# Performance work log

Measured on AMD Instinct MI355X. Metric: run time of the kernel, lower is better.

Reference implementation:

```python
import jax, jax.numpy as jnp
import numpy as np

N = 50000
E = 800000
IN_C, HID_C, OUT_C = 128, 256, 2


def sage_conv(x, src, dst, W_l, b_l, W_r, num_nodes):
    # PyG SAGEConv with mean aggregation:
    #   out = lin_l(mean_{j in N(i)} x_j) + lin_r(x_i)
    msg = x[src]                                            # [E, d] gather
    agg = jax.ops.segment_sum(msg, dst, num_segments=num_nodes)   # [N, d]
    cnt = jax.ops.segment_sum(jnp.ones((msg.shape[0],), x.dtype), dst,
                              num_segments=num_nodes)        # [N]
    agg = agg / jnp.maximum(cnt, 1.0)[:, None]               # mean (deg>=1)
    return agg @ W_l.T + b_l + x @ W_r.T


def setup_inputs() -> dict:
    key = jax.random.key(0)
    ks = jax.random.split(key, 8)
    x = jax.random.normal(ks[0], (N, IN_C), dtype=jnp.float32)
    edge_index = jax.random.randint(ks[1], (2, E), 0, N, dtype=jnp.int32)
    # glorot-ish scaled params
    s1 = 1.0 / np.sqrt(IN_C)
    s2 = 1.0 / np.sqrt(HID_C)
    W1l = jax.random.normal(ks[2], (HID_C, IN_C), dtype=jnp.float32) * s1
    W1r = jax.random.normal(ks[3], (HID_C, IN_C), dtype=jnp.float32) * s1
    b1 = jnp.zeros((HID_C,), dtype=jnp.float32)
    W2l = jax.random.normal(ks[4], (OUT_C, HID_C), dtype=jnp.float32) * s2
    W2r = jax.random.normal(ks[5], (OUT_C, HID_C), dtype=jnp.float32) * s2
    b2 = jnp.zeros((OUT_C,), dtype=jnp.float32)
    return {"x": x, "edge_index": edge_index,
            "W1l": W1l, "b1": b1, "W1r": W1r,
            "W2l": W2l, "b2": b2, "W2r": W2r}


def reference(x, edge_index, W1l, b1, W1r, W2l, b2, W2r):
    src, dst = edge_index[0], edge_index[1]
    h = sage_conv(x, src, dst, W1l, b1, W1r, N)
    h = jax.nn.relu(h)
    out = sage_conv(h, src, dst, W2l, b2, W2r, N)
    return out
```

## Files before the change

### kernel.cpp

```cpp
#include <hip/hip_runtime.h>
#include <hip/hip_bf16.h>


#define IN_C 128
#define HID_C 256
#define BKT_SHIFT 7
#define BKT_W 128
#define MAX_BKT_E 4096

typedef __attribute__((ext_vector_type(8))) short short8;
typedef __attribute__((ext_vector_type(4))) float f32x4;

static __device__ __forceinline__ unsigned short f2b(float f) {
    __hip_bfloat16 h = __float2bfloat16(f);
    return *(unsigned short*)&h;
}
static __device__ __forceinline__ float b2f(unsigned short u) {
    unsigned v = ((unsigned)u) << 16;
    return *(float*)&v;
}


__global__ __launch_bounds__(256) void bin_count(const int* __restrict__ ei,
                                                 int* __restrict__ bhist, int E_) {
    __shared__ int hist[512];
    const int tid = threadIdx.x;
    for (int i = tid; i < 512; i += 256) hist[i] = 0;
    __syncthreads();
    const int e0 = blockIdx.x * 2048;
#pragma unroll
    for (int j = 0; j < 8; ++j) {
        int e = e0 + j * 256 + tid;
        if (e < E_) atomicAdd(&hist[ei[E_ + e] >> BKT_SHIFT], 1);
    }
    __syncthreads();
    for (int i = tid; i < 512; i += 256) {
        int c = hist[i];
        if (c) atomicAdd(&bhist[i], c);
    }
}

__global__ __launch_bounds__(512) void bin_scan(const int* __restrict__ bhist,
                                                int* __restrict__ bbase,
                                                int* __restrict__ bcursor,
                                                int* __restrict__ rowptr,
                                                int nbkt, int n, int E_) {
    __shared__ int wsum[8];
    const int tid = threadIdx.x;
    const int lane = tid & 63;
    const int wid = tid >> 6;
    int v = (tid < nbkt) ? bhist[tid] : 0;
    int incl = v;
#pragma unroll
    for (int off = 1; off < 64; off <<= 1) {
        int t = __shfl_up(incl, off);
        if (lane >= off) incl += t;
    }
    if (lane == 63) wsum[wid] = incl;
    __syncthreads();
    int woff = 0;
    for (int w = 0; w < 8; ++w)
        if (w < wid) woff += wsum[w];
    int excl = woff + incl - v;
    if (tid < nbkt) { bbase[tid] = excl; bcursor[tid] = excl; }
    if (tid == 511) { bbase[nbkt] = woff + incl; rowptr[n] = E_; }
}

__global__ __launch_bounds__(256) void bin_scatter(const int* __restrict__ ei,
                                                   int* __restrict__ bcursor,
                                                   unsigned int* __restrict__ binned,
                                                   int E_) {
    __shared__ int hist[512];
    __shared__ int lbase[512];
    const int tid = threadIdx.x;
    const int e0 = blockIdx.x * 4096;
    for (int i = tid; i < 512; i += 256) hist[i] = 0;
    __syncthreads();
#pragma unroll
    for (int j = 0; j < 16; ++j) {
        int e = e0 + j * 256 + tid;
        if (e < E_) atomicAdd(&hist[ei[E_ + e] >> BKT_SHIFT], 1);
    }
    __syncthreads();
    for (int i = tid; i < 512; i += 256) {
        int c = hist[i];
        lbase[i] = c ? atomicAdd(&bcursor[i], c) : 0;
        hist[i] = 0;
    }
    __syncthreads();
#pragma unroll
    for (int j = 0; j < 16; ++j) {
        int e = e0 + j * 256 + tid;
        if (e < E_) {
            int d = ei[E_ + e];
            int b = d >> BKT_SHIFT;
            int pos = lbase[b] + atomicAdd(&hist[b], 1);
            binned[pos] = ((unsigned)ei[e] << BKT_SHIFT) | (unsigned)(d & (BKT_W - 1));
        }
    }
}

__global__ __launch_bounds__(256) void fine_sort(const unsigned int* __restrict__ binned,
                                                 const int* __restrict__ bbase,
                                                 int* __restrict__ rowptr,
                                                 int* __restrict__ elist, int n) {
    __shared__ unsigned int ebuf[MAX_BKT_E];
    __shared__ unsigned short sbuf[MAX_BKT_E];
    __shared__ int hist[BKT_W];
    __shared__ int offs[BKT_W];
    __shared__ int cur[BKT_W];
    const int tid = threadIdx.x;
    const int lane = tid & 63;
    const int bkt = blockIdx.x;
    const int gbase = bbase[bkt];
    int cnt = bbase[bkt + 1] - gbase;
    if (cnt > MAX_BKT_E) cnt = MAX_BKT_E;

    if (tid < BKT_W) hist[tid] = 0;
    for (int i = tid; i < cnt; i += 256) ebuf[i] = binned[gbase + i];
    __syncthreads();
    for (int i = tid; i < cnt; i += 256)
        atomicAdd(&hist[ebuf[i] & (BKT_W - 1)], 1);
    __syncthreads();
    if (tid < 64) {
        int h0 = hist[lane * 2], h1 = hist[lane * 2 + 1];
        int s = h0 + h1;
        int incl = s;
#pragma unroll
        for (int off = 1; off < 64; off <<= 1) {
            int t = __shfl_up(incl, off);
            if (lane >= off) incl += t;
        }
        int excl = incl - s;
        offs[lane * 2] = excl;         cur[lane * 2] = excl;
        offs[lane * 2 + 1] = excl + h0; cur[lane * 2 + 1] = excl + h0;
    }
    __syncthreads();
    if (tid < BKT_W) {
        int d = bkt * BKT_W + tid;
        if (d < n) rowptr[d] = gbase + offs[tid];
    }
    for (int i = tid; i < cnt; i += 256) {
        unsigned int pk = ebuf[i];
        int pos = atomicAdd(&cur[pk & (BKT_W - 1)], 1);
        sbuf[pos] = (unsigned short)(pk >> BKT_SHIFT);
    }
    __syncthreads();
    for (int i = tid; i < cnt; i += 256)
        elist[gbase + i] = (int)sbuf[i];
}


__global__ void convert_all(const float* __restrict__ x, unsigned int* __restrict__ xh,
                            unsigned int* __restrict__ Abf,
                            const float* __restrict__ w1l, const float* __restrict__ w1r,
                            unsigned short* __restrict__ Bg,
                            int npairs , int xblk) {
    if (blockIdx.x < xblk) {
        int t = blockIdx.x * 256 + threadIdx.x;
        if (t >= npairs) return;
        float2 v = *(const float2*)&x[(size_t)t * 2];
        unsigned int o = ((unsigned)f2b(v.y) << 16) | f2b(v.x);
        xh[t] = o;
        int node = t >> 6, g = t & 63;
        Abf[(size_t)node * 128 + 64 + g] = o;
    } else {
        int idx = (blockIdx.x - xblk) * 256 + threadIdx.x;
        int o = idx >> 8, k = idx & 255;
        float f = (k < IN_C) ? w1l[o * IN_C + k] : w1r[o * IN_C + (k - IN_C)];
        Bg[idx] = f2b(f);
    }
}


__global__ __launch_bounds__(256) void gather_agg1(
    const int* __restrict__ rowptr, const int* __restrict__ elist,
    const uint4* __restrict__ xh4, uint4* __restrict__ Abf4, int n) {
    int node = blockIdx.x * 4 + (threadIdx.x >> 6);
    int lane = threadIdx.x & 63;
    if (node >= n) return;
    const int ep = lane >> 4;
    const int pos = lane & 15;
    int beg = rowptr[node], end = rowptr[node + 1];

    float s[8] = {0.f, 0.f, 0.f, 0.f, 0.f, 0.f, 0.f, 0.f};
    for (int e = beg; e < end; e += 8) {
        int e0 = e + ep;
        int e1 = e + 4 + ep;
        if (e0 < end) {
            uint4 u = xh4[(size_t)elist[e0] * 16 + pos];
            s[0] += b2f(u.x & 0xffff); s[1] += b2f(u.x >> 16);
            s[2] += b2f(u.y & 0xffff); s[3] += b2f(u.y >> 16);
            s[4] += b2f(u.z & 0xffff); s[5] += b2f(u.z >> 16);
            s[6] += b2f(u.w & 0xffff); s[7] += b2f(u.w >> 16);
        }
        if (e1 < end) {
            uint4 u = xh4[(size_t)elist[e1] * 16 + pos];
            s[0] += b2f(u.x & 0xffff); s[1] += b2f(u.x >> 16);
            s[2] += b2f(u.y & 0xffff); s[3] += b2f(u.y >> 16);
            s[4] += b2f(u.z & 0xffff); s[5] += b2f(u.z >> 16);
            s[6] += b2f(u.w & 0xffff); s[7] += b2f(u.w >> 16);
        }
    }
#pragma unroll
    for (int i = 0; i < 8; ++i) {
        s[i] += __shfl_xor(s[i], 16);
        s[i] += __shfl_xor(s[i], 32);
    }
    if (ep == 0) {
        float inv = 1.0f / (float)max(end - beg, 1);
        uint4 o;
        o.x = ((unsigned)f2b(s[1] * inv) << 16) | f2b(s[0] * inv);
        o.y = ((unsigned)f2b(s[3] * inv) << 16) | f2b(s[2] * inv);
        o.z = ((unsigned)f2b(s[5] * inv) << 16) | f2b(s[4] * inv);
        o.w = ((unsigned)f2b(s[7] * inv) << 16) | f2b(s[6] * inv);
        Abf4[(size_t)node * 32 + pos] = o;
    }
}


#define LSTR 72

__global__ __launch_bounds__(256) void gemm1_fused(
    const unsigned short* __restrict__ Abf, const unsigned short* __restrict__ Bg,
    const float* __restrict__ b1, const float* __restrict__ w2l,
    const float* __restrict__ w2r, float* __restrict__ pr_part, int nn) {
    __shared__ short As[128 * LSTR];
    __shared__ short Bs[128 * LSTR];

    const int tid = threadIdx.x;
    const int lane = tid & 63;
    const int wid = tid >> 6;
    const int wm = wid >> 1, wn = wid & 1;
    const int row0 = blockIdx.x * 128;
    const int col0 = blockIdx.y * 128;

    const int srow = tid >> 1;
    const int skc = (tid & 1) * 32;
    int arow = row0 + srow;
    if (arow >= nn) arow = nn - 1;
    const size_t agoff = (size_t)arow * 256 + skc;
    const size_t bgoff = (size_t)(col0 + srow) * 256 + skc;

    f32x4 acc[4][4];
#pragma unroll
    for (int i = 0; i < 4; ++i)
#pragma unroll
        for (int j = 0; j < 4; ++j) acc[i][j] = (f32x4){0.f, 0.f, 0.f, 0.f};

    const int quad = lane >> 4;
    const int l16 = lane & 15;

    for (int k0 = 0; k0 < 256; k0 += 64) {
        const uint4* ga = (const uint4*)(Abf + agoff + k0);
        const uint4* gb = (const uint4*)(Bg + bgoff + k0);
        uint4 va0 = ga[0], va1 = ga[1], va2 = ga[2], va3 = ga[3];
        uint4 vb0 = gb[0], vb1 = gb[1], vb2 = gb[2], vb3 = gb[3];

        __syncthreads();
        uint4* la = (uint4*)&As[srow * LSTR + skc];
        uint4* lb = (uint4*)&Bs[srow * LSTR + skc];
        la[0] = va0; la[1] = va1; la[2] = va2; la[3] = va3;
        lb[0] = vb0; lb[1] = vb1; lb[2] = vb2; lb[3] = vb3;
        __syncthreads();

#pragma unroll
        for (int kb = 0; kb < 2; ++kb) {
            short8 af[4], bf[4];
#pragma unroll
            for (int mt = 0; mt < 4; ++mt)
                af[mt] = *(const short8*)&As[(wm * 64 + mt * 16 + l16) * LSTR + kb * 32 + quad * 8];
#pragma unroll
            for (int nt = 0; nt < 4; ++nt)
                bf[nt] = *(const short8*)&Bs[(wn * 64 + nt * 16 + l16) * LSTR + kb * 32 + quad * 8];
#pragma unroll
            for (int mt = 0; mt < 4; ++mt)
#pragma unroll
                for (int nt = 0; nt < 4; ++nt)
                    acc[mt][nt] = __builtin_amdgcn_mfma_f32_16x16x32_bf16(
                        af[mt], bf[nt], acc[mt][nt], 0, 0, 0);
        }
    }

    const int cbase = col0 + wn * 64 + l16;
    const int cby = blockIdx.y * 2 + wn;
#pragma unroll
    for (int half = 0; half < 2; ++half) {
        const float* wA = half ? w2r : w2l;
        f32x4 part[2][4];
#pragma unroll
        for (int c = 0; c < 2; ++c)
#pragma unroll
            for (int mt = 0; mt < 4; ++mt) part[c][mt] = (f32x4){0.f, 0.f, 0.f, 0.f};
#pragma unroll
        for (int nt = 0; nt < 4; ++nt) {
            const int col = cbase + nt * 16;
            const float bias = b1[col];
            const float w0 = wA[col];
            const float w1 = wA[HID_C + col];
#pragma unroll
            for (int mt = 0; mt < 4; ++mt)
#pragma unroll
                for (int r = 0; r < 4; ++r) {
                    float hv = fmaxf(acc[mt][nt][r] + bias, 0.0f);
                    part[0][mt][r] += hv * w0;
                    part[1][mt][r] += hv * w1;
                }
        }
#pragma unroll
        for (int c = 0; c < 2; ++c)
#pragma unroll
            for (int mt = 0; mt < 4; ++mt)
#pragma unroll
                for (int r = 0; r < 4; ++r)
#pragma unroll
                    for (int m = 1; m < 16; m <<= 1)
                        part[c][mt][r] += __shfl_xor(part[c][mt][r], m);
        if (l16 < 8) {
            const int ch2 = l16 & 1;
            const int mts = l16 >> 1;
#pragma unroll
            for (int r = 0; r < 4; ++r) {
                int row = row0 + wm * 64 + quad * 4 + mts * 16 + r;
                if (row < nn)
                    pr_part[(size_t)row * 16 + cby * 4 + half * 2 + ch2] =
                        part[ch2][mts][r];
            }
        }
    }
}


__global__ void combine2(const float* __restrict__ pr_part,
                         float2* __restrict__ p2, float2* __restrict__ rs, int n) {
    int i = blockIdx.x * 256 + threadIdx.x;
    if (i >= n) return;
    const float4* q = (const float4*)(pr_part + (size_t)i * 16);
    float4 a = q[0], b = q[1], c = q[2], d = q[3];
    p2[i] = make_float2(a.x + b.x + c.x + d.x, a.y + b.y + c.y + d.y);
    rs[i] = make_float2(a.z + b.z + c.z + d.z, a.w + b.w + c.w + d.w);
}

__global__ void gather_fin(const int* __restrict__ rowptr, const int* __restrict__ elist,
                           const float2* __restrict__ p2, const float2* __restrict__ rs,
                           const float* __restrict__ b2, float* __restrict__ out, int n) {
    int i = blockIdx.x * 256 + threadIdx.x;
    if (i >= n) return;
    int beg = rowptr[i], end = rowptr[i + 1];
    float s0 = 0.0f, s1 = 0.0f;
    for (int e = beg; e < end; ++e) {
        float2 v = p2[elist[e]];
        s0 += v.x; s1 += v.y;
    }
    float inv = 1.0f / (float)max(end - beg, 1);
    float2 self = rs[i];
    out[i * 2 + 0] = s0 * inv + self.x + b2[0];
    out[i * 2 + 1] = s1 * inv + self.y + b2[1];
}


extern "C" void kernel_launch(void* const* d_in, const int* in_sizes, int n_in,
                              void* d_out, int out_size, void* d_ws, size_t ws_size,
                              hipStream_t stream) {
    const float* x   = (const float*)d_in[0];
    const int*   ei  = (const int*)d_in[1];
    const float* W1l = (const float*)d_in[2];
    const float* b1  = (const float*)d_in[3];
    const float* W1r = (const float*)d_in[4];
    const float* W2l = (const float*)d_in[5];
    const float* b2  = (const float*)d_in[6];
    const float* W2r = (const float*)d_in[7];
    float* out = (float*)d_out;

    const int N_ = in_sizes[0] / IN_C;
    const int E_ = in_sizes[1] / 2;
    const int nbkt = (N_ + BKT_W - 1) / BKT_W;

    char* wsb = (char*)d_ws;
    size_t off = 0;
    auto alloc = [&](size_t bytes) {
        void* ptr = wsb + off;
        off += ((bytes + 15) & ~(size_t)15);
        return ptr;
    };
    unsigned short* Abf = (unsigned short*)alloc((size_t)N_ * 256 * 2);
    unsigned int*   xh  = (unsigned int*)alloc((size_t)N_ * 64 * 4);
    unsigned short* Bg  = (unsigned short*)alloc(256 * 256 * 2);
    float* pr_part = (float*)alloc((size_t)N_ * 16 * 4);
    int*   rowptr = (int*)alloc((size_t)(N_ + 1) * 4);
    int*   elist  = (int*)alloc((size_t)E_ * 4);
    unsigned int* binned = (unsigned int*)alloc((size_t)E_ * 4);
    int*   bhist  = (int*)alloc(512 * 4);
    int*   bbase  = (int*)alloc(513 * 4);
    int*   bcursor= (int*)alloc(512 * 4);
    float2* p2 = (float2*)alloc((size_t)N_ * 2 * 4);
    float2* rs = (float2*)alloc((size_t)N_ * 2 * 4);

    const int xblk = (N_ * 64 + 255) / 256;

    hipMemsetAsync(bhist, 0, 512 * sizeof(int), stream);
    bin_count<<<(E_ + 2047) / 2048, 256, 0, stream>>>(ei, bhist, E_);
    convert_all<<<xblk + 256, 256, 0, stream>>>(x, xh, (unsigned int*)Abf,
                                                W1l, W1r, Bg, N_ * 64, xblk);
    bin_scan<<<1, 512, 0, stream>>>(bhist, bbase, bcursor, rowptr, nbkt, N_, E_);
    bin_scatter<<<(E_ + 4095) / 4096, 256, 0, stream>>>(ei, bcursor, binned, E_);
    fine_sort<<<nbkt, 256, 0, stream>>>(binned, bbase, rowptr, elist, N_);

    gather_agg1<<<(N_ + 3) / 4, 256, 0, stream>>>(rowptr, elist,
                                                  (const uint4*)xh, (uint4*)Abf, N_);
    gemm1_fused<<<dim3((N_ + 127) / 128, 2), 256, 0, stream>>>(
        Abf, Bg, b1, W2l, W2r, pr_part, N_);

    combine2<<<(N_ + 255) / 256, 256, 0, stream>>>(pr_part, p2, rs, N_);
    gather_fin<<<(N_ + 255) / 256, 256, 0, stream>>>(rowptr, elist, p2, rs, b2, out, N_);
}
```

Measured before the change: 219.3 us.

## Replace CSR fine sort with per-bucket shared-memory atomic aggregation

```diff
diff --git a/kernel.cpp b/kernel.cpp
--- a/kernel.cpp
+++ b/kernel.cpp
@@ -6,7 +6,6 @@
 #define HID_C 256
 #define BKT_SHIFT 7
 #define BKT_W 128
-#define MAX_BKT_E 4096
 
 typedef __attribute__((ext_vector_type(8))) short short8;
 typedef __attribute__((ext_vector_type(4))) float f32x4;
@@ -43,8 +42,7 @@
 __global__ __launch_bounds__(512) void bin_scan(const int* __restrict__ bhist,
                                                 int* __restrict__ bbase,
                                                 int* __restrict__ bcursor,
-                                                int* __restrict__ rowptr,
-                                                int nbkt, int n, int E_) {
+                                                int nbkt) {
     __shared__ int wsum[8];
     const int tid = threadIdx.x;
     const int lane = tid & 63;
@@ -63,7 +61,7 @@
         if (w < wid) woff += wsum[w];
     int excl = woff + incl - v;
     if (tid < nbkt) { bbase[tid] = excl; bcursor[tid] = excl; }
-    if (tid == 511) { bbase[nbkt] = woff + incl; rowptr[n] = E_; }
+    if (tid == 511) bbase[nbkt] = woff + incl;
 }
 
 __global__ __launch_bounds__(256) void bin_scatter(const int* __restrict__ ei,
@@ -98,56 +96,6 @@
             binned[pos] = ((unsigned)ei[e] << BKT_SHIFT) | (unsigned)(d & (BKT_W - 1));
         }
     }
-}
-
-__global__ __launch_bounds__(256) void fine_sort(const unsigned int* __restrict__ binned,
-                                                 const int* __restrict__ bbase,
-                                                 int* __restrict__ rowptr,
-                                                 int* __restrict__ elist, int n) {
-    __shared__ unsigned int ebuf[MAX_BKT_E];
-    __shared__ unsigned short sbuf[MAX_BKT_E];
-    __shared__ int hist[BKT_W];
-    __shared__ int offs[BKT_W];
-    __shared__ int cur[BKT_W];
-    const int tid = threadIdx.x;
-    const int lane = tid & 63;
-    const int bkt = blockIdx.x;
-    const int gbase = bbase[bkt];
-    int cnt = bbase[bkt + 1] - gbase;
-    if (cnt > MAX_BKT_E) cnt = MAX_BKT_E;
-
-    if (tid < BKT_W) hist[tid] = 0;
-    for (int i = tid; i < cnt; i += 256) ebuf[i] = binned[gbase + i];
-    __syncthreads();
-    for (int i = tid; i < cnt; i += 256)
-        atomicAdd(&hist[ebuf[i] & (BKT_W - 1)], 1);
-    __syncthreads();
-    if (tid < 64) {
-        int h0 = hist[lane * 2], h1 = hist[lane * 2 + 1];
-        int s = h0 + h1;
-        int incl = s;
-#pragma unroll
-        for (int off = 1; off < 64; off <<= 1) {
-            int t = __shfl_up(incl, off);
-            if (lane >= off) incl += t;
-        }
-        int excl = incl - s;
-        offs[lane * 2] = excl;         cur[lane * 2] = excl;
-        offs[lane * 2 + 1] = excl + h0; cur[lane * 2 + 1] = excl + h0;
-    }
-    __syncthreads();
-    if (tid < BKT_W) {
-        int d = bkt * BKT_W + tid;
-        if (d < n) rowptr[d] = gbase + offs[tid];
-    }
-    for (int i = tid; i < cnt; i += 256) {
-        unsigned int pk = ebuf[i];
-        int pos = atomicAdd(&cur[pk & (BKT_W - 1)], 1);
-        sbuf[pos] = (unsigned short)(pk >> BKT_SHIFT);
-    }
-    __syncthreads();
-    for (int i = tid; i < cnt; i += 256)
-        elist[gbase + i] = (int)sbuf[i];
 }
 
 
@@ -173,48 +121,57 @@
 }
 
 
-__global__ __launch_bounds__(256) void gather_agg1(
-    const int* __restrict__ rowptr, const int* __restrict__ elist,
-    const uint4* __restrict__ xh4, uint4* __restrict__ Abf4, int n) {
-    int node = blockIdx.x * 4 + (threadIdx.x >> 6);
-    int lane = threadIdx.x & 63;
-    if (node >= n) return;
-    const int ep = lane >> 4;
-    const int pos = lane & 15;
-    int beg = rowptr[node], end = rowptr[node + 1];
-
-    float s[8] = {0.f, 0.f, 0.f, 0.f, 0.f, 0.f, 0.f, 0.f};
-    for (int e = beg; e < end; e += 8) {
-        int e0 = e + ep;
-        int e1 = e + 4 + ep;
-        if (e0 < end) {
-            uint4 u = xh4[(size_t)elist[e0] * 16 + pos];
-            s[0] += b2f(u.x & 0xffff); s[1] += b2f(u.x >> 16);
-            s[2] += b2f(u.y & 0xffff); s[3] += b2f(u.y >> 16);
-            s[4] += b2f(u.z & 0xffff); s[5] += b2f(u.z >> 16);
-            s[6] += b2f(u.w & 0xffff); s[7] += b2f(u.w >> 16);
-        }
-        if (e1 < end) {
-            uint4 u = xh4[(size_t)elist[e1] * 16 + pos];
-            s[0] += b2f(u.x & 0xffff); s[1] += b2f(u.x >> 16);
-            s[2] += b2f(u.y & 0xffff); s[3] += b2f(u.y >> 16);
-            s[4] += b2f(u.z & 0xffff); s[5] += b2f(u.z >> 16);
-            s[6] += b2f(u.w & 0xffff); s[7] += b2f(u.w >> 16);
-        }
-    }
-#pragma unroll
-    for (int i = 0; i < 8; ++i) {
-        s[i] += __shfl_xor(s[i], 16);
-        s[i] += __shfl_xor(s[i], 32);
-    }
-    if (ep == 0) {
-        float inv = 1.0f / (float)max(end - beg, 1);
-        uint4 o;
-        o.x = ((unsigned)f2b(s[1] * inv) << 16) | f2b(s[0] * inv);
-        o.y = ((unsigned)f2b(s[3] * inv) << 16) | f2b(s[2] * inv);
-        o.z = ((unsigned)f2b(s[5] * inv) << 16) | f2b(s[4] * inv);
-        o.w = ((unsigned)f2b(s[7] * inv) << 16) | f2b(s[6] * inv);
-        Abf4[(size_t)node * 32 + pos] = o;
+__global__ __launch_bounds__(256) void agg1_bucket(
+    const unsigned int* __restrict__ binned, const int* __restrict__ bbase,
+    const unsigned int* __restrict__ xh, unsigned int* __restrict__ Abf,
+    int* __restrict__ deg, int n) {
+    __shared__ float acc[BKT_W * 128];
+    __shared__ int dcnt[BKT_W];
+    const int tid = threadIdx.x;
+    const int lane = tid & 63;
+    const int wv = tid >> 6;
+    const int bkt = blockIdx.x;
+    const int gbase = bbase[bkt];
+    const int gend = bbase[bkt + 1];
+
+    for (int i = tid; i < BKT_W * 128; i += 256) acc[i] = 0.0f;
+    if (tid < BKT_W) dcnt[tid] = 0;
+    __syncthreads();
+
+    for (int e = gbase + wv * 2; e < gend; e += 8) {
+        {
+            unsigned pk = binned[e];
+            int src = pk >> BKT_SHIFT, dl = pk & (BKT_W - 1);
+            unsigned u = xh[(size_t)src * 64 + lane];
+            float* a = &acc[dl * 128];
+            atomicAdd(&a[2 * lane],     b2f(u & 0xffff));
+            atomicAdd(&a[2 * lane + 1], b2f(u >> 16));
+            if (lane == 0) atomicAdd(&dcnt[dl], 1);
+        }
+        if (e + 1 < gend) {
+            unsigned pk = binned[e + 1];
+            int src = pk >> BKT_SHIFT, dl = pk & (BKT_W - 1);
+            unsigned u = xh[(size_t)src * 64 + lane];
+            float* a = &acc[dl * 128];
+            atomicAdd(&a[2 * lane],     b2f(u & 0xffff));
+            atomicAdd(&a[2 * lane + 1], b2f(u >> 16));
+            if (lane == 0) atomicAdd(&dcnt[dl], 1);
+        }
+    }
+    __syncthreads();
+
+    for (int r = wv; r < BKT_W; r += 4) {
+        int node = bkt * BKT_W + r;
+        if (node < n) {
+            float inv = 1.0f / (float)max(dcnt[r], 1);
+            float f0 = acc[r * 128 + 2 * lane]     * inv;
+            float f1 = acc[r * 128 + 2 * lane + 1] * inv;
+            Abf[(size_t)node * 128 + lane] = ((unsigned)f2b(f1) << 16) | f2b(f0);
+        }
+    }
+    if (tid < BKT_W) {
+        int node = bkt * BKT_W + tid;
+        if (node < n) deg[node] = dcnt[tid];
     }
 }
 
@@ -341,21 +298,35 @@
     rs[i] = make_float2(a.z + b.z + c.z + d.z, a.w + b.w + c.w + d.w);
 }
 
-__global__ void gather_fin(const int* __restrict__ rowptr, const int* __restrict__ elist,
-                           const float2* __restrict__ p2, const float2* __restrict__ rs,
-                           const float* __restrict__ b2, float* __restrict__ out, int n) {
-    int i = blockIdx.x * 256 + threadIdx.x;
-    if (i >= n) return;
-    int beg = rowptr[i], end = rowptr[i + 1];
-    float s0 = 0.0f, s1 = 0.0f;
-    for (int e = beg; e < end; ++e) {
-        float2 v = p2[elist[e]];
-        s0 += v.x; s1 += v.y;
-    }
-    float inv = 1.0f / (float)max(end - beg, 1);
-    float2 self = rs[i];
-    out[i * 2 + 0] = s0 * inv + self.x + b2[0];
-    out[i * 2 + 1] = s1 * inv + self.y + b2[1];
+__global__ __launch_bounds__(256) void fin_bucket(
+    const unsigned int* __restrict__ binned, const int* __restrict__ bbase,
+    const float2* __restrict__ p2, const float2* __restrict__ rs,
+    const int* __restrict__ deg, const float* __restrict__ b2,
+    float* __restrict__ out, int n) {
+    __shared__ float a0[BKT_W];
+    __shared__ float a1[BKT_W];
+    const int tid = threadIdx.x;
+    const int bkt = blockIdx.x;
+    const int gbase = bbase[bkt];
+    const int cnt = bbase[bkt + 1] - gbase;
+    if (tid < BKT_W) { a0[tid] = 0.0f; a1[tid] = 0.0f; }
+    __syncthreads();
+    for (int i = tid; i < cnt; i += 256) {
+        unsigned pk = binned[gbase + i];
+        float2 v = p2[pk >> BKT_SHIFT];
+        atomicAdd(&a0[pk & (BKT_W - 1)], v.x);
+        atomicAdd(&a1[pk & (BKT_W - 1)], v.y);
+    }
+    __syncthreads();
+    if (tid < BKT_W) {
+        int node = bkt * BKT_W + tid;
+        if (node < n) {
+            float inv = 1.0f / (float)max(deg[node], 1);
+            float2 self = rs[node];
+            out[node * 2 + 0] = a0[tid] * inv + self.x + b2[0];
+            out[node * 2 + 1] = a1[tid] * inv + self.y + b2[1];
+        }
+    }
 }
 
 
@@ -387,9 +358,8 @@
     unsigned int*   xh  = (unsigned int*)alloc((size_t)N_ * 64 * 4);
     unsigned short* Bg  = (unsigned short*)alloc(256 * 256 * 2);
     float* pr_part = (float*)alloc((size_t)N_ * 16 * 4);
-    int*   rowptr = (int*)alloc((size_t)(N_ + 1) * 4);
-    int*   elist  = (int*)alloc((size_t)E_ * 4);
     unsigned int* binned = (unsigned int*)alloc((size_t)E_ * 4);
+    int*   deg    = (int*)alloc((size_t)N_ * 4);
     int*   bhist  = (int*)alloc(512 * 4);
     int*   bbase  = (int*)alloc(513 * 4);
     int*   bcursor= (int*)alloc(512 * 4);
@@ -402,15 +372,14 @@
     bin_count<<<(E_ + 2047) / 2048, 256, 0, stream>>>(ei, bhist, E_);
     convert_all<<<xblk + 256, 256, 0, stream>>>(x, xh, (unsigned int*)Abf,
                                                 W1l, W1r, Bg, N_ * 64, xblk);
-    bin_scan<<<1, 512, 0, stream>>>(bhist, bbase, bcursor, rowptr, nbkt, N_, E_);
+    bin_scan<<<1, 512, 0, stream>>>(bhist, bbase, bcursor, nbkt);
     bin_scatter<<<(E_ + 4095) / 4096, 256, 0, stream>>>(ei, bcursor, binned, E_);
-    fine_sort<<<nbkt, 256, 0, stream>>>(binned, bbase, rowptr, elist, N_);
-
-    gather_agg1<<<(N_ + 3) / 4, 256, 0, stream>>>(rowptr, elist,
-                                                  (const uint4*)xh, (uint4*)Abf, N_);
+
+    agg1_bucket<<<nbkt, 256, 0, stream>>>(binned, bbase, xh, (unsigned int*)Abf,
+                                          deg, N_);
     gemm1_fused<<<dim3((N_ + 127) / 128, 2), 256, 0, stream>>>(
         Abf, Bg, b1, W2l, W2r, pr_part, N_);
 
     combine2<<<(N_ + 255) / 256, 256, 0, stream>>>(pr_part, p2, rs, N_);
-    gather_fin<<<(N_ + 255) / 256, 256, 0, stream>>>(rowptr, elist, p2, rs, b2, out, N_);
-}
+    fin_bucket<<<nbkt, 256, 0, stream>>>(binned, bbase, p2, rs, deg, b2, out, N_);
+}
```

Result: slower. 874.8 us (+298.9%).
